# Optimization experiments

Hardware: AMD Instinct MI355X
Metric: run time of the kernel (lower is better)

Reference implementation:

```python
import jax, jax.numpy as jnp
import numpy as np
from jax import lax

B, S = 256, 512
CHAR_NUM, CLASS_NUM, OUTPUT_NUM, WORD_EMBED, H = 10, 10, 64, 32, 128
EPS = 1e-12


def setup_inputs() -> dict:
    key = jax.random.key(0)
    ks = jax.random.split(key, 16)
    def nrm(k, shape, s=0.05):
        return jax.random.normal(k, shape, dtype=jnp.float32) * s
    return {
        "char_ids": jax.random.randint(ks[0], (B, S), 0, CHAR_NUM),
        "word_ids": jax.random.randint(ks[1], (B, S), 0, CHAR_NUM),
        "subject_ids": jax.random.randint(ks[2], (B, 2), 0, S),
        "emb_char": nrm(ks[3], (CHAR_NUM, OUTPUT_NUM)),
        "emb_word": nrm(ks[4], (CHAR_NUM, WORD_EMBED)),
        "Wwc": nrm(ks[5], (WORD_EMBED, OUTPUT_NUM)),
        "bwc": jnp.zeros((OUTPUT_NUM,), jnp.float32),
        "l1_Wx": nrm(ks[6], (OUTPUT_NUM, 4 * H)),
        "l1_Wh": nrm(ks[7], (H, 4 * H)),
        "l1_b": jnp.zeros((4 * H,), jnp.float32),
        "l2_Wx": nrm(ks[8], (H, 4 * H)),
        "l2_Wh": nrm(ks[9], (H, 4 * H)),
        "l2_b": jnp.zeros((4 * H,), jnp.float32),
        "beta_W": nrm(ks[10], (2 * H, H)),
        "beta_b": jnp.zeros((H,), jnp.float32),
        "gamma_W": nrm(ks[11], (2 * H, H)),
        "gamma_b": jnp.zeros((H,), jnp.float32),
        "sub_W": nrm(ks[12], (H, 2)),
        "sub_b": jnp.zeros((2,), jnp.float32),
        "po_W": nrm(ks[13], (H, 2 * CLASS_NUM)),
        "po_b": jnp.zeros((2 * CLASS_NUM,), jnp.float32),
    }


def _lstm_cell(x, h, c, Wx, Wh, b):
    # Keras LSTMCell: gates ordered i, f, g(cell), o
    z = x @ Wx + h @ Wh + b
    i, f, g, o = jnp.split(z, 4, axis=-1)
    c_new = jax.nn.sigmoid(f) * c + jax.nn.sigmoid(i) * jnp.tanh(g)
    h_new = jax.nn.sigmoid(o) * jnp.tanh(c_new)
    return h_new, c_new


def reference(char_ids, word_ids, subject_ids,
              emb_char, emb_word, Wwc, bwc,
              l1_Wx, l1_Wh, l1_b, l2_Wx, l2_Wh, l2_b,
              beta_W, beta_b, gamma_W, gamma_b,
              sub_W, sub_b, po_W, po_b):
    b, s = char_ids.shape
    # NOTE: source passes mask = (char_ids == 0) to the RNN; in Keras, mask True
    # means the step IS processed, so only positions with id==0 update state.
    step_mask = (char_ids == 0)  # [B, S] bool

    emb = emb_char[char_ids] + (emb_word[word_ids] @ Wwc + bwc)  # [B, S, 64]

    def step(carry, inp):
        h1, c1, h2, c2 = carry
        xt, mt = inp  # xt [B, 64], mt [B]
        h1n, c1n = _lstm_cell(xt, h1, c1, l1_Wx, l1_Wh, l1_b)
        h2n, c2n = _lstm_cell(h1n, h2, c2, l2_Wx, l2_Wh, l2_b)
        m = mt[:, None]
        h1 = jnp.where(m, h1n, h1)
        c1 = jnp.where(m, c1n, c1)
        h2 = jnp.where(m, h2n, h2)
        c2 = jnp.where(m, c2n, c2)
        return (h1, c1, h2, c2), h2

    z = jnp.zeros((b, H), emb.dtype)
    _, outs = lax.scan(step, (z, z, z, z),
                       (emb.transpose(1, 0, 2), step_mask.T))
    sent = outs.transpose(1, 0, 2)  # [B, S, 128]

    # vectorized batch_gather (replaces eager numpy per-row loop)
    bidx = jnp.arange(b)
    sub_start = sent[bidx, subject_ids[:, 0]]  # [B, 128]
    sub_end = sent[bidx, subject_ids[:, 1]]    # [B, 128]
    subject = jnp.concatenate([sub_start, sub_end], axis=1)  # [B, 256]

    # conditional layer norm
    beta = subject @ beta_W + beta_b    # [B, 128]
    gamma = subject @ gamma_W + gamma_b
    u = jnp.mean(sent, axis=-1, keepdims=True)
    v = jnp.mean((sent - u) ** 2, axis=-1, keepdims=True)
    xhat = (sent - u) / jnp.sqrt(v + EPS)
    context = gamma[:, None, :] * xhat + beta[:, None, :]  # [B, S, 128]

    # (transformer_encoder LSTM(32) output is dead code in the source; omitted)
    sub_preds = sent @ sub_W + sub_b                     # [B, S, 2]
    po_preds = (context @ po_W + po_b).reshape(b, -1, CLASS_NUM, 2)  # [B, S, 10, 2]
    return sub_preds, po_preds
```

## Files before the change

### kernel.cpp

```cpp
#include <hip/hip_runtime.h>
#include <cstdint>
#include <cstddef>


#define HIST 128
#define HPAD 132

typedef _Float16 f16x8 __attribute__((ext_vector_type(8)));
typedef float    f32x4 __attribute__((ext_vector_type(4)));

__device__ __forceinline__ f16x8 as_h8(const uint4& v) {
    f16x8 r; __builtin_memcpy(&r, &v, 16); return r;
}

#define MFMA16(a, b, c) __builtin_amdgcn_mfma_f32_16x16x32_f16((a), (b), (c), 0, 0, 0)

__device__ __forceinline__ float fast_rcp(float x) {
#if __has_builtin(__builtin_amdgcn_rcpf)
    return __builtin_amdgcn_rcpf(x);
#else
    return 1.f / x;
#endif
}
__device__ __forceinline__ float sigm(float x) {
    x = fminf(fmaxf(x, -30.f), 30.f);
    return fast_rcp(1.f + __expf(-x));
}
__device__ __forceinline__ float tanh_fast(float x) {
    x = fminf(fmaxf(x, -15.f), 15.f);
    float e = __expf(-2.f * x);
    return (1.f - e) * fast_rcp(1.f + e);
}

__global__ __launch_bounds__(512) void k_prep(
    const float* __restrict__ emb_char, const float* __restrict__ emb_word,
    const float* __restrict__ Wwc, const float* __restrict__ bwc,
    const float* __restrict__ l1_Wx, const float* __restrict__ l1_b,
    const float* __restrict__ l1_Wh, const float* __restrict__ l2_Wx,
    const float* __restrict__ l2_Wh,
    float* __restrict__ XW1, uint4* __restrict__ WF)
{
    const int blk = blockIdx.x;
    const int T = threadIdx.x;
    if (blk < 10) {
        __shared__ float xw[64];
        if (T < 64) {
            float acc = emb_char[T] + bwc[T];
            for (int m = 0; m < 32; ++m) acc += emb_word[blk * 32 + m] * Wwc[m * 64 + T];
            xw[T] = acc;
        }
        __syncthreads();
        float acc = l1_b[T];
        for (int k = 0; k < 64; ++k) acc += xw[k] * l1_Wx[k * 512 + T];
        XW1[blk * 512 + T] = acc;
    } else {
        const int gid = (blk - 10) * 512 + T;
        const int thr = gid / 48;
        const int f   = gid - thr * 48;
        const int w   = thr >> 6, l = thr & 63;
        const int kb  = 8 * (l >> 4);
        const bool isL2 = (f < 32);
        int j, ks;
        if (isL2) { j = f >> 3; ks = f & 7; }
        else      { const int f2 = f - 32; j = f2 >> 2; ks = f2 & 3; }
        const int col = j * 128 + 16 * w + (l & 15);
        union { uint4 qv; _Float16 h[8]; } o;
        for (int e = 0; e < 8; ++e) {
            const int k = ks * 32 + kb + e;
            float v;
            if (isL2) v = (k < 128) ? l2_Wh[k * 512 + col] : l2_Wx[(k - 128) * 512 + col];
            else      v = l1_Wh[k * 512 + col];
            o.h[e] = (_Float16)v;
        }
        WF[gid] = o.qv;
    }
}

__global__ __launch_bounds__(512, 2) void k_lstm(
    const int* __restrict__ char_ids, const int* __restrict__ word_ids,
    const int* __restrict__ subject_ids,
    const float* __restrict__ XW1, const uint4* __restrict__ WF,
    const float* __restrict__ l2_b,
    const float* __restrict__ beta_W, const float* __restrict__ beta_b,
    const float* __restrict__ gamma_W, const float* __restrict__ gamma_b,
    const float* __restrict__ sub_W, const float* __restrict__ sub_b,
    const float* __restrict__ po_W, const float* __restrict__ po_b,
    float* __restrict__ out)
{
    const int b    = blockIdx.x;
    const int T    = threadIdx.x;
    const int lane = T & 63;
    const int wv   = T >> 6;
    const int kb   = 8 * (lane >> 4);
    const int unit = 16 * wv + (lane & 15);
    const bool g16 = (lane < 16);

    __shared__ int   charL[512];
    __shared__ int   wordL[512];
    __shared__ float XW1L[5120];
    __shared__ __align__(16) _Float16 hcat[2][256];
    __shared__ short wlist[512];
    __shared__ unsigned short idxL[512];
    __shared__ int   ccnt[8];
    __shared__ __align__(16) float hl[HIST * HPAD];
    __shared__ float A[20][132];
    __shared__ float K1[20], K2[20];
    __shared__ float gm[128], bt[128];
    __shared__ float urs[HIST][2];
    __shared__ float povals[HIST * 20];
    __shared__ float subv[HIST * 2];
    __shared__ float swl[256];
    __shared__ float subj[256];

    charL[T] = char_ids[b * 512 + T];
    wordL[T] = word_ids[b * 512 + T];
#pragma unroll
    for (int i = 0; i < 10; ++i) XW1L[i * 512 + T] = XW1[i * 512 + T];
    __syncthreads();

    const bool act = (charL[T] == 0);
    const unsigned long long bmask = __ballot(act);
    if (lane == 0) ccnt[wv] = (int)__popcll(bmask);
    __syncthreads();
    int base = 0;
    for (int i = 0; i < wv; ++i) base += ccnt[i];
    int tot = base;
    for (int i = wv; i < 8; ++i) tot += ccnt[i];
    if (act) {
        const int pos = base + (int)__popcll(bmask & ((1ull << lane) - 1ull));
        wlist[pos] = (short)wordL[T];
    }
    {
        const int cin = base + (int)__popcll(bmask & ((2ull << lane) - 1ull));
        idxL[T] = (unsigned short)(cin < HIST - 1 ? cin : HIST - 1);
    }
    const int nact = tot;

    if (T < 128) {
        hcat[0][T] = (_Float16)0.f;
        hl[T]      = 0.f;
    }
    float c1 = 0.f, c2 = 0.f;
    const float l2b0 = l2_b[unit];
    const float l2b1 = l2_b[128 + unit];
    const float l2b2 = l2_b[256 + unit];
    const float l2b3 = l2_b[384 + unit];

    uint4 wf[48];
    {
        const uint4* p = WF + (size_t)T * 48;
#pragma unroll
        for (int i = 0; i < 48; ++i) wf[i] = p[i];
    }
    __syncthreads();

    if (nact > 0) {
        const int w0_ = wlist[0];
        const float zi = XW1L[w0_ * 512 + unit];
        const float zg = XW1L[w0_ * 512 + 256 + unit];
        const float zo = XW1L[w0_ * 512 + 384 + unit];
        c1 = sigm(zi) * tanh_fast(zg);
        const float h1n = sigm(zo) * tanh_fast(c1);
        if (g16) hcat[0][128 + unit] = (_Float16)h1n;
        __syncthreads();
    }

    int cur = 0;
    for (int a = 0; a < nact; ++a) {
        const _Float16* hc = hcat[cur];
        _Float16*       hn = hcat[cur ^ 1];

        f32x4 acc0 = {l2b0, 0.f, 0.f, 0.f};
        f32x4 acc1 = {l2b1, 0.f, 0.f, 0.f};
        f32x4 acc2 = {l2b2, 0.f, 0.f, 0.f};
        f32x4 acc3 = {l2b3, 0.f, 0.f, 0.f};
#pragma unroll
        for (int ks = 0; ks < 8; ++ks) {
            const f16x8 aa = *(const f16x8*)&hc[kb + 32 * ks];
            acc0 = MFMA16(aa, as_h8(wf[0 * 8 + ks]), acc0);
            acc1 = MFMA16(aa, as_h8(wf[1 * 8 + ks]), acc1);
            acc2 = MFMA16(aa, as_h8(wf[2 * 8 + ks]), acc2);
            acc3 = MFMA16(aa, as_h8(wf[3 * 8 + ks]), acc3);
        }
        if (g16) {
            c2 = sigm(acc1[0]) * c2 + sigm(acc0[0]) * tanh_fast(acc2[0]);
            const float h2v = sigm(acc3[0]) * tanh_fast(c2);
            hn[unit] = (_Float16)h2v;
            const int slot = (a + 1 < HIST - 1) ? a + 1 : HIST - 1;
            hl[slot * HPAD + unit] = h2v;
        }

        if (a + 1 < nact) {
            const int wid = wlist[a + 1];
            f32x4 r0 = {XW1L[wid * 512 + unit],       0.f, 0.f, 0.f};
            f32x4 r1 = {XW1L[wid * 512 + 128 + unit], 0.f, 0.f, 0.f};
            f32x4 r2 = {XW1L[wid * 512 + 256 + unit], 0.f, 0.f, 0.f};
            f32x4 r3 = {XW1L[wid * 512 + 384 + unit], 0.f, 0.f, 0.f};
#pragma unroll
            for (int ks = 0; ks < 4; ++ks) {
                const f16x8 aa = *(const f16x8*)&hc[128 + kb + 32 * ks];
                r0 = MFMA16(aa, as_h8(wf[32 + 0 * 4 + ks]), r0);
                r1 = MFMA16(aa, as_h8(wf[32 + 1 * 4 + ks]), r1);
                r2 = MFMA16(aa, as_h8(wf[32 + 2 * 4 + ks]), r2);
                r3 = MFMA16(aa, as_h8(wf[32 + 3 * 4 + ks]), r3);
            }
            if (g16) {
                c1 = sigm(r1[0]) * c1 + sigm(r0[0]) * tanh_fast(r2[0]);
                const float h1n = sigm(r3[0]) * tanh_fast(c1);
                hn[128 + unit] = (_Float16)h1n;
            }
        }
        __syncthreads();
        cur ^= 1;
    }

    if (T < 256) {
        swl[T] = sub_W[T];
        const int uu = T & 127, half = T >> 7;
        const int sidx = subject_ids[b * 2 + half];
        const int slot = idxL[sidx];
        subj[T] = hl[slot * HPAD + uu];
    }
    __syncthreads();

    if (T < 256) {
        const int uu = T & 127, half = T >> 7;
        const float* __restrict__ W = half ? gamma_W : beta_W;
        float acc = half ? gamma_b[uu] : beta_b[uu];
        for (int c = 0; c < 256; ++c) acc += subj[c] * W[c * 128 + uu];
        if (half) gm[uu] = acc;
        else      bt[uu] = acc;
    }
    __syncthreads();

    for (int i = T; i < 2560; i += 512) {
        const int o = i >> 7, c = i & 127;
        A[o][c] = gm[c] * po_W[c * 20 + o];
    }
    if (T < 20) {
        float k1 = po_b[T], k2 = 0.f;
        for (int c = 0; c < 128; ++c) {
            const float pw = po_W[c * 20 + T];
            k1 += bt[c] * pw;
            k2 += gm[c] * pw;
        }
        K1[T] = k1; K2[T] = k2;
    }
    const int nslot = (int)idxL[511] + 1;
    const float sb0 = sub_b[0], sb1 = sub_b[1];
    for (int s = T; s < nslot; s += 512) {
        const float4* hp4 = (const float4*)&hl[s * HPAD];
        float sum = 0.f, s2 = 0.f, sub0 = sb0, sub1 = sb1;
        for (int c4 = 0; c4 < 32; ++c4) {
            const float4 h = hp4[c4];
            sum += (h.x + h.y) + (h.z + h.w);
            s2  += h.x * h.x + h.y * h.y + h.z * h.z + h.w * h.w;
            const int c = 4 * c4;
            sub0 += h.x * swl[2 * c] + h.y * swl[2 * c + 2] + h.z * swl[2 * c + 4] + h.w * swl[2 * c + 6];
            sub1 += h.x * swl[2 * c + 1] + h.y * swl[2 * c + 3] + h.z * swl[2 * c + 5] + h.w * swl[2 * c + 7];
        }
        const float mu = sum * (1.f / 128.f);
        const float vv = fmaxf(s2 * (1.f / 128.f) - mu * mu, 0.f);
        urs[s][0] = mu;
        urs[s][1] = 1.f / sqrtf(vv + 1e-12f);
        subv[2 * s] = sub0; subv[2 * s + 1] = sub1;
    }
    __syncthreads();

    for (int i = T; i < nslot * 20; i += 512) {
        const int s = i / 20, o = i - 20 * s;
        const float mu = urs[s][0], rs = urs[s][1];
        const float4* hp4 = (const float4*)&hl[s * HPAD];
        const float* Ao = &A[o][0];
        float acc = 0.f;
        for (int c4 = 0; c4 < 32; ++c4) {
            const float4 h = hp4[c4];
            const float4 aa = *(const float4*)&Ao[4 * c4];
            acc += h.x * aa.x + h.y * aa.y + h.z * aa.z + h.w * aa.w;
        }
        povals[i] = rs * acc - mu * rs * K2[o] + K1[o];
    }
    __syncthreads();

    for (int i = T; i < 2560; i += 512) {
        const int t = i / 5, j = i - 5 * t;
        const int sl = idxL[t];
        const float4 v = *(const float4*)&povals[sl * 20 + 4 * j];
        *(float4*)&out[262144 + ((size_t)(b * 512 + t)) * 20 + 4 * j] = v;
    }
    for (int i = T; i < 512; i += 512) {
        const int sl = idxL[i];
        float2 v; v.x = subv[2 * sl]; v.y = subv[2 * sl + 1];
        *(float2*)&out[((size_t)(b * 512 + i)) * 2] = v;
    }
}

extern "C" void kernel_launch(void* const* d_in, const int* in_sizes, int n_in,
                              void* d_out, int out_size, void* d_ws, size_t ws_size,
                              hipStream_t stream) {
    (void)in_sizes; (void)n_in; (void)out_size; (void)ws_size;
    const int*   char_ids    = (const int*)d_in[0];
    const int*   word_ids    = (const int*)d_in[1];
    const int*   subject_ids = (const int*)d_in[2];
    const float* emb_char    = (const float*)d_in[3];
    const float* emb_word    = (const float*)d_in[4];
    const float* Wwc         = (const float*)d_in[5];
    const float* bwc         = (const float*)d_in[6];
    const float* l1_Wx       = (const float*)d_in[7];
    const float* l1_b        = (const float*)d_in[9];
    const float* l1_Wh       = (const float*)d_in[8];
    const float* l2_Wx       = (const float*)d_in[10];
    const float* l2_Wh       = (const float*)d_in[11];
    const float* l2_b        = (const float*)d_in[12];
    const float* beta_W      = (const float*)d_in[13];
    const float* beta_b      = (const float*)d_in[14];
    const float* gamma_W     = (const float*)d_in[15];
    const float* gamma_b     = (const float*)d_in[16];
    const float* sub_W       = (const float*)d_in[17];
    const float* sub_b       = (const float*)d_in[18];
    const float* po_W        = (const float*)d_in[19];
    const float* po_b        = (const float*)d_in[20];
    float* out = (float*)d_out;

    char* ws = (char*)d_ws;
    float* XW1 = (float*)(ws + 0);
    uint4* WF  = (uint4*)(ws + 32768);

    k_prep<<<dim3(58), dim3(512), 0, stream>>>(emb_char, emb_word, Wwc, bwc,
                                               l1_Wx, l1_b, l1_Wh, l2_Wx, l2_Wh,
                                               XW1, WF);
    k_lstm<<<dim3(256), dim3(512), 0, stream>>>(char_ids, word_ids, subject_ids,
                                                XW1, WF, l2_b,
                                                beta_W, beta_b, gamma_W, gamma_b,
                                                sub_W, sub_b, po_W, po_b, out);
}
```

Measured before the change: 203.3 us.

## Halve LSTM block to 4 waves, each wave computing two hidden-unit groups

The recurrent kernel now runs 256 threads (4 waves) per batch row instead of 512. Each wave handles 32 hidden units through two MFMA column groups, and each thread holds 96 fp16 weight fragments, pinned to AGPRs with inline asm. The prep kernel's weight packing is changed to match the new fragment layout. The aim is to cut cross-wave barrier cost and wave count in the serial recurrence, at the cost of more MFMAs per wave per step and higher register pressure.

```diff
diff --git a/kernel.cpp b/kernel.cpp
--- a/kernel.cpp
+++ b/kernel.cpp
@@ -55,28 +55,28 @@
         XW1[blk * 512 + T] = acc;
     } else {
         const int gid = (blk - 10) * 512 + T;
-        const int thr = gid / 48;
-        const int f   = gid - thr * 48;
+        const int thr = gid / 96;
+        const int f   = gid - thr * 96;
         const int w   = thr >> 6, l = thr & 63;
         const int kb  = 8 * (l >> 4);
-        const bool isL2 = (f < 32);
-        int j, ks;
-        if (isL2) { j = f >> 3; ks = f & 7; }
-        else      { const int f2 = f - 32; j = f2 >> 2; ks = f2 & 3; }
-        const int col = j * 128 + 16 * w + (l & 15);
-        union { uint4 qv; _Float16 h[8]; } o;
+        const bool isL2 = (f < 96 - 32);
+        int j, h, ks;
+        if (isL2) { j = f >> 4; h = (f >> 3) & 1; ks = f & 7; }
+        else      { const int f2 = f - 64; j = f2 >> 3; h = (f2 >> 2) & 1; ks = f2 & 3; }
+        const int col = j * 128 + 32 * w + 16 * h + (l & 15);
+        union { uint4 qv; _Float16 hh[8]; } o;
         for (int e = 0; e < 8; ++e) {
             const int k = ks * 32 + kb + e;
             float v;
             if (isL2) v = (k < 128) ? l2_Wh[k * 512 + col] : l2_Wx[(k - 128) * 512 + col];
             else      v = l1_Wh[k * 512 + col];
-            o.h[e] = (_Float16)v;
+            o.hh[e] = (_Float16)v;
         }
         WF[gid] = o.qv;
     }
 }
 
-__global__ __launch_bounds__(512, 2) void k_lstm(
+__global__ __launch_bounds__(256, 1) void k_lstm(
     const int* __restrict__ char_ids, const int* __restrict__ word_ids,
     const int* __restrict__ subject_ids,
     const float* __restrict__ XW1, const uint4* __restrict__ WF,
@@ -91,9 +91,11 @@
     const int T    = threadIdx.x;
     const int lane = T & 63;
     const int wv   = T >> 6;
+    const int l15  = lane & 15;
     const int kb   = 8 * (lane >> 4);
-    const int unit = 16 * wv + (lane & 15);
     const bool g16 = (lane < 16);
+    const int u0   = 32 * wv + l15;
+    const int u1   = u0 + 16;
 
     __shared__ int   charL[512];
     __shared__ int   wordL[512];
@@ -112,56 +114,66 @@
     __shared__ float swl[256];
     __shared__ float subj[256];
 
-    charL[T] = char_ids[b * 512 + T];
-    wordL[T] = word_ids[b * 512 + T];
-#pragma unroll
-    for (int i = 0; i < 10; ++i) XW1L[i * 512 + T] = XW1[i * 512 + T];
-    __syncthreads();
-
-    const bool act = (charL[T] == 0);
-    const unsigned long long bmask = __ballot(act);
-    if (lane == 0) ccnt[wv] = (int)__popcll(bmask);
-    __syncthreads();
-    int base = 0;
-    for (int i = 0; i < wv; ++i) base += ccnt[i];
-    int tot = base;
-    for (int i = wv; i < 8; ++i) tot += ccnt[i];
-    if (act) {
-        const int pos = base + (int)__popcll(bmask & ((1ull << lane) - 1ull));
-        wlist[pos] = (short)wordL[T];
-    }
+    charL[T]       = char_ids[b * 512 + T];
+    charL[256 + T] = char_ids[b * 512 + 256 + T];
+    wordL[T]       = word_ids[b * 512 + T];
+    wordL[256 + T] = word_ids[b * 512 + 256 + T];
+    for (int i = T; i < 5120; i += 256) XW1L[i] = XW1[i];
+    __syncthreads();
+
+    const bool act0 = (charL[T] == 0);
+    const bool act1 = (charL[256 + T] == 0);
+    const unsigned long long bm0 = __ballot(act0);
+    const unsigned long long bm1 = __ballot(act1);
+    if (lane == 0) { ccnt[wv] = (int)__popcll(bm0); ccnt[4 + wv] = (int)__popcll(bm1); }
+    __syncthreads();
+    int baseC[8];
+    int tot = 0;
+    for (int i = 0; i < 8; ++i) { baseC[i] = tot; tot += ccnt[i]; }
+    const int nact = tot;
+    if (act0) wlist[baseC[wv]     + (int)__popcll(bm0 & ((1ull << lane) - 1ull))] = (short)wordL[T];
+    if (act1) wlist[baseC[4 + wv] + (int)__popcll(bm1 & ((1ull << lane) - 1ull))] = (short)wordL[256 + T];
     {
-        const int cin = base + (int)__popcll(bmask & ((2ull << lane) - 1ull));
-        idxL[T] = (unsigned short)(cin < HIST - 1 ? cin : HIST - 1);
-    }
-    const int nact = tot;
+        const int c0 = baseC[wv]     + (int)__popcll(bm0 & ((2ull << lane) - 1ull));
+        const int c1 = baseC[4 + wv] + (int)__popcll(bm1 & ((2ull << lane) - 1ull));
+        idxL[T]       = (unsigned short)(c0 < HIST - 1 ? c0 : HIST - 1);
+        idxL[256 + T] = (unsigned short)(c1 < HIST - 1 ? c1 : HIST - 1);
+    }
 
     if (T < 128) {
         hcat[0][T] = (_Float16)0.f;
         hl[T]      = 0.f;
     }
-    float c1 = 0.f, c2 = 0.f;
-    const float l2b0 = l2_b[unit];
-    const float l2b1 = l2_b[128 + unit];
-    const float l2b2 = l2_b[256 + unit];
-    const float l2b3 = l2_b[384 + unit];
-
-    uint4 wf[48];
+    float c1_0 = 0.f, c1_1 = 0.f, c2_0 = 0.f, c2_1 = 0.f;
+    const float l2b00 = l2_b[u0],       l2b01 = l2_b[u1];
+    const float l2b10 = l2_b[128 + u0], l2b11 = l2_b[128 + u1];
+    const float l2b20 = l2_b[256 + u0], l2b21 = l2_b[256 + u1];
+    const float l2b30 = l2_b[384 + u0], l2b31 = l2_b[384 + u1];
+
+    uint4 wf[96];
     {
-        const uint4* p = WF + (size_t)T * 48;
+        const uint4* p = WF + (size_t)T * 96;
 #pragma unroll
-        for (int i = 0; i < 48; ++i) wf[i] = p[i];
-    }
+        for (int i = 0; i < 96; ++i) wf[i] = p[i];
+    }
+#pragma unroll
+    for (int i = 0; i < 96; ++i)
+        asm volatile("" : "+a"(wf[i].x), "+a"(wf[i].y), "+a"(wf[i].z), "+a"(wf[i].w));
     __syncthreads();
 
     if (nact > 0) {
         const int w0_ = wlist[0];
-        const float zi = XW1L[w0_ * 512 + unit];
-        const float zg = XW1L[w0_ * 512 + 256 + unit];
-        const float zo = XW1L[w0_ * 512 + 384 + unit];
-        c1 = sigm(zi) * tanh_fast(zg);
-        const float h1n = sigm(zo) * tanh_fast(c1);
-        if (g16) hcat[0][128 + unit] = (_Float16)h1n;
+        const float zi0 = XW1L[w0_ * 512 + u0],       zi1 = XW1L[w0_ * 512 + u1];
+        const float zg0 = XW1L[w0_ * 512 + 256 + u0], zg1 = XW1L[w0_ * 512 + 256 + u1];
+        const float zo0 = XW1L[w0_ * 512 + 384 + u0], zo1 = XW1L[w0_ * 512 + 384 + u1];
+        c1_0 = sigm(zi0) * tanh_fast(zg0);
+        c1_1 = sigm(zi1) * tanh_fast(zg1);
+        const float h1n0 = sigm(zo0) * tanh_fast(c1_0);
+        const float h1n1 = sigm(zo1) * tanh_fast(c1_1);
+        if (g16) {
+            hcat[0][128 + u0] = (_Float16)h1n0;
+            hcat[0][128 + u1] = (_Float16)h1n1;
+        }
         __syncthreads();
     }
 
@@ -170,51 +182,67 @@
         const _Float16* hc = hcat[cur];
         _Float16*       hn = hcat[cur ^ 1];
 
-        f32x4 acc0 = {l2b0, 0.f, 0.f, 0.f};
-        f32x4 acc1 = {l2b1, 0.f, 0.f, 0.f};
-        f32x4 acc2 = {l2b2, 0.f, 0.f, 0.f};
-        f32x4 acc3 = {l2b3, 0.f, 0.f, 0.f};
+        f32x4 q00 = {l2b00, 0.f, 0.f, 0.f}, q01 = {l2b01, 0.f, 0.f, 0.f};
+        f32x4 q10 = {l2b10, 0.f, 0.f, 0.f}, q11 = {l2b11, 0.f, 0.f, 0.f};
+        f32x4 q20 = {l2b20, 0.f, 0.f, 0.f}, q21 = {l2b21, 0.f, 0.f, 0.f};
+        f32x4 q30 = {l2b30, 0.f, 0.f, 0.f}, q31 = {l2b31, 0.f, 0.f, 0.f};
 #pragma unroll
         for (int ks = 0; ks < 8; ++ks) {
             const f16x8 aa = *(const f16x8*)&hc[kb + 32 * ks];
-            acc0 = MFMA16(aa, as_h8(wf[0 * 8 + ks]), acc0);
-            acc1 = MFMA16(aa, as_h8(wf[1 * 8 + ks]), acc1);
-            acc2 = MFMA16(aa, as_h8(wf[2 * 8 + ks]), acc2);
-            acc3 = MFMA16(aa, as_h8(wf[3 * 8 + ks]), acc3);
+            q00 = MFMA16(aa, as_h8(wf[ 0 + ks]), q00);
+            q01 = MFMA16(aa, as_h8(wf[ 8 + ks]), q01);
+            q10 = MFMA16(aa, as_h8(wf[16 + ks]), q10);
+            q11 = MFMA16(aa, as_h8(wf[24 + ks]), q11);
+            q20 = MFMA16(aa, as_h8(wf[32 + ks]), q20);
+            q21 = MFMA16(aa, as_h8(wf[40 + ks]), q21);
+            q30 = MFMA16(aa, as_h8(wf[48 + ks]), q30);
+            q31 = MFMA16(aa, as_h8(wf[56 + ks]), q31);
         }
         if (g16) {
-            c2 = sigm(acc1[0]) * c2 + sigm(acc0[0]) * tanh_fast(acc2[0]);
-            const float h2v = sigm(acc3[0]) * tanh_fast(c2);
-            hn[unit] = (_Float16)h2v;
+            c2_0 = sigm(q10[0]) * c2_0 + sigm(q00[0]) * tanh_fast(q20[0]);
+            const float h2v0 = sigm(q30[0]) * tanh_fast(c2_0);
+            c2_1 = sigm(q11[0]) * c2_1 + sigm(q01[0]) * tanh_fast(q21[0]);
+            const float h2v1 = sigm(q31[0]) * tanh_fast(c2_1);
+            hn[u0] = (_Float16)h2v0;
+            hn[u1] = (_Float16)h2v1;
             const int slot = (a + 1 < HIST - 1) ? a + 1 : HIST - 1;
-            hl[slot * HPAD + unit] = h2v;
+            hl[slot * HPAD + u0] = h2v0;
+            hl[slot * HPAD + u1] = h2v1;
         }
 
         if (a + 1 < nact) {
             const int wid = wlist[a + 1];
-            f32x4 r0 = {XW1L[wid * 512 + unit],       0.f, 0.f, 0.f};
-            f32x4 r1 = {XW1L[wid * 512 + 128 + unit], 0.f, 0.f, 0.f};
-            f32x4 r2 = {XW1L[wid * 512 + 256 + unit], 0.f, 0.f, 0.f};
-            f32x4 r3 = {XW1L[wid * 512 + 384 + unit], 0.f, 0.f, 0.f};
+            const float* xb = &XW1L[wid * 512];
+            f32x4 r00 = {xb[u0],       0.f, 0.f, 0.f}, r01 = {xb[u1],       0.f, 0.f, 0.f};
+            f32x4 r10 = {xb[128 + u0], 0.f, 0.f, 0.f}, r11 = {xb[128 + u1], 0.f, 0.f, 0.f};
+            f32x4 r20 = {xb[256 + u0], 0.f, 0.f, 0.f}, r21 = {xb[256 + u1], 0.f, 0.f, 0.f};
+            f32x4 r30 = {xb[384 + u0], 0.f, 0.f, 0.f}, r31 = {xb[384 + u1], 0.f, 0.f, 0.f};
 #pragma unroll
             for (int ks = 0; ks < 4; ++ks) {
                 const f16x8 aa = *(const f16x8*)&hc[128 + kb + 32 * ks];
-                r0 = MFMA16(aa, as_h8(wf[32 + 0 * 4 + ks]), r0);
-                r1 = MFMA16(aa, as_h8(wf[32 + 1 * 4 + ks]), r1);
-                r2 = MFMA16(aa, as_h8(wf[32 + 2 * 4 + ks]), r2);
-                r3 = MFMA16(aa, as_h8(wf[32 + 3 * 4 + ks]), r3);
+                r00 = MFMA16(aa, as_h8(wf[64 + 0 + ks]), r00);
+                r01 = MFMA16(aa, as_h8(wf[64 + 4 + ks]), r01);
+                r10 = MFMA16(aa, as_h8(wf[64 + 8 + ks]), r10);
+                r11 = MFMA16(aa, as_h8(wf[64 + 12 + ks]), r11);
+                r20 = MFMA16(aa, as_h8(wf[64 + 16 + ks]), r20);
+                r21 = MFMA16(aa, as_h8(wf[64 + 20 + ks]), r21);
+                r30 = MFMA16(aa, as_h8(wf[64 + 24 + ks]), r30);
+                r31 = MFMA16(aa, as_h8(wf[64 + 28 + ks]), r31);
             }
             if (g16) {
-                c1 = sigm(r1[0]) * c1 + sigm(r0[0]) * tanh_fast(r2[0]);
-                const float h1n = sigm(r3[0]) * tanh_fast(c1);
-                hn[128 + unit] = (_Float16)h1n;
+                c1_0 = sigm(r10[0]) * c1_0 + sigm(r00[0]) * tanh_fast(r20[0]);
+                const float h1n0 = sigm(r30[0]) * tanh_fast(c1_0);
+                c1_1 = sigm(r11[0]) * c1_1 + sigm(r01[0]) * tanh_fast(r21[0]);
+                const float h1n1 = sigm(r31[0]) * tanh_fast(c1_1);
+                hn[128 + u0] = (_Float16)h1n0;
+                hn[128 + u1] = (_Float16)h1n1;
             }
         }
         __syncthreads();
         cur ^= 1;
     }
 
-    if (T < 256) {
+    {
         swl[T] = sub_W[T];
         const int uu = T & 127, half = T >> 7;
         const int sidx = subject_ids[b * 2 + half];
@@ -223,7 +251,7 @@
     }
     __syncthreads();
 
-    if (T < 256) {
+    {
         const int uu = T & 127, half = T >> 7;
         const float* __restrict__ W = half ? gamma_W : beta_W;
         float acc = half ? gamma_b[uu] : beta_b[uu];
@@ -233,7 +261,7 @@
     }
     __syncthreads();
 
-    for (int i = T; i < 2560; i += 512) {
+    for (int i = T; i < 2560; i += 256) {
         const int o = i >> 7, c = i & 127;
         A[o][c] = gm[c] * po_W[c * 20 + o];
     }
@@ -248,7 +276,7 @@
     }
     const int nslot = (int)idxL[511] + 1;
     const float sb0 = sub_b[0], sb1 = sub_b[1];
-    for (int s = T; s < nslot; s += 512) {
+    for (int s = T; s < nslot; s += 256) {
         const float4* hp4 = (const float4*)&hl[s * HPAD];
         float sum = 0.f, s2 = 0.f, sub0 = sb0, sub1 = sb1;
         for (int c4 = 0; c4 < 32; ++c4) {
@@ -267,7 +295,7 @@
     }
     __syncthreads();
 
-    for (int i = T; i < nslot * 20; i += 512) {
+    for (int i = T; i < nslot * 20; i += 256) {
         const int s = i / 20, o = i - 20 * s;
         const float mu = urs[s][0], rs = urs[s][1];
         const float4* hp4 = (const float4*)&hl[s * HPAD];
@@ -282,13 +310,13 @@
     }
     __syncthreads();
 
-    for (int i = T; i < 2560; i += 512) {
+    for (int i = T; i < 2560; i += 256) {
         const int t = i / 5, j = i - 5 * t;
         const int sl = idxL[t];
         const float4 v = *(const float4*)&povals[sl * 20 + 4 * j];
         *(float4*)&out[262144 + ((size_t)(b * 512 + t)) * 20 + 4 * j] = v;
     }
-    for (int i = T; i < 512; i += 512) {
+    for (int i = T; i < 512; i += 256) {
         const int sl = idxL[i];
         float2 v; v.x = subv[2 * sl]; v.y = subv[2 * sl + 1];
         *(float2*)&out[((size_t)(b * 512 + i)) * 2] = v;
@@ -307,8 +335,8 @@
     const float* Wwc         = (const float*)d_in[5];
     const float* bwc         = (const float*)d_in[6];
     const float* l1_Wx       = (const float*)d_in[7];
+    const float* l1_Wh       = (const float*)d_in[8];
     const float* l1_b        = (const float*)d_in[9];
-    const float* l1_Wh       = (const float*)d_in[8];
     const float* l2_Wx       = (const float*)d_in[10];
     const float* l2_Wh       = (const float*)d_in[11];
     const float* l2_b        = (const float*)d_in[12];
@@ -329,7 +357,7 @@
     k_prep<<<dim3(58), dim3(512), 0, stream>>>(emb_char, emb_word, Wwc, bwc,
                                                l1_Wx, l1_b, l1_Wh, l2_Wx, l2_Wh,
                                                XW1, WF);
-    k_lstm<<<dim3(256), dim3(512), 0, stream>>>(char_ids, word_ids, subject_ids,
+    k_lstm<<<dim3(256), dim3(256), 0, stream>>>(char_ids, word_ids, subject_ids,
                                                 XW1, WF, l2_b,
                                                 beta_W, beta_b, gamma_W, gamma_b,
                                                 sub_W, sub_b, po_W, po_b, out);
```

Result: slower. 252.5 us (+24.2%).

## Specialize waves: separate layer-1 and layer-2 LSTM waves in a 768-thread block

Applied to the files above, without the earlier changes.

The block grows from 8 to 12 waves. Eight waves compute only the layer-2 gates and four waves compute only the layer-1 gates, with each layer-1 wave covering two 16-unit groups, so both layers' matrix products run at the same time instead of one after the other inside each wave. The weight-packing kernel is rewritten so that each thread holds 32 register fragments instead of 48, which lowers register pressure, and an empty asm statement keeps the weights in vector registers. The intent is to shorten the serial per-timestep MFMA chain on the recurrence critical path. In exchange the block launches more waves, and layer-1 waves still run two dependent 16-MFMA chains back to back.

```diff
diff --git a/kernel.cpp b/kernel.cpp
--- a/kernel.cpp
+++ b/kernel.cpp
@@ -55,28 +55,33 @@
         XW1[blk * 512 + T] = acc;
     } else {
         const int gid = (blk - 10) * 512 + T;
-        const int thr = gid / 48;
-        const int f   = gid - thr * 48;
+        const int thr = gid >> 5;
+        const int f   = gid & 31;
         const int w   = thr >> 6, l = thr & 63;
         const int kb  = 8 * (l >> 4);
-        const bool isL2 = (f < 32);
-        int j, ks;
-        if (isL2) { j = f >> 3; ks = f & 7; }
-        else      { const int f2 = f - 32; j = f2 >> 2; ks = f2 & 3; }
-        const int col = j * 128 + 16 * w + (l & 15);
-        union { uint4 qv; _Float16 h[8]; } o;
-        for (int e = 0; e < 8; ++e) {
-            const int k = ks * 32 + kb + e;
-            float v;
-            if (isL2) v = (k < 128) ? l2_Wh[k * 512 + col] : l2_Wx[(k - 128) * 512 + col];
-            else      v = l1_Wh[k * 512 + col];
-            o.h[e] = (_Float16)v;
+        union { uint4 qv; _Float16 hh[8]; } o;
+        if (w < 8) {
+            const int j = f >> 3, ks = f & 7;
+            const int col = j * 128 + 16 * w + (l & 15);
+            for (int e = 0; e < 8; ++e) {
+                const int k = ks * 32 + kb + e;
+                o.hh[e] = (_Float16)((k < 128) ? l2_Wh[k * 512 + col]
+                                               : l2_Wx[(k - 128) * 512 + col]);
+            }
+        } else {
+            const int w1 = w - 8;
+            const int j = f >> 3, h = (f >> 2) & 1, ks = f & 3;
+            const int col = j * 128 + 32 * w1 + 16 * h + (l & 15);
+            for (int e = 0; e < 8; ++e) {
+                const int k = ks * 32 + kb + e;
+                o.hh[e] = (_Float16)l1_Wh[k * 512 + col];
+            }
         }
         WF[gid] = o.qv;
     }
 }
 
-__global__ __launch_bounds__(512, 2) void k_lstm(
+__global__ __launch_bounds__(768, 3) void k_lstm(
     const int* __restrict__ char_ids, const int* __restrict__ word_ids,
     const int* __restrict__ subject_ids,
     const float* __restrict__ XW1, const uint4* __restrict__ WF,
@@ -91,9 +96,14 @@
     const int T    = threadIdx.x;
     const int lane = T & 63;
     const int wv   = T >> 6;
+    const int l15  = lane & 15;
     const int kb   = 8 * (lane >> 4);
-    const int unit = 16 * wv + (lane & 15);
     const bool g16 = (lane < 16);
+    const bool isL2 = (wv < 8);
+    const int u2   = 16 * (wv & 7) + l15;
+    const int w1   = wv - 8;
+    const int u0   = 32 * (w1 & 3) + l15;
+    const int u1   = u0 + 16;
 
     __shared__ int   charL[512];
     __shared__ int   wordL[512];
@@ -112,56 +122,67 @@
     __shared__ float swl[256];
     __shared__ float subj[256];
 
-    charL[T] = char_ids[b * 512 + T];
-    wordL[T] = word_ids[b * 512 + T];
-#pragma unroll
-    for (int i = 0; i < 10; ++i) XW1L[i * 512 + T] = XW1[i * 512 + T];
-    __syncthreads();
-
-    const bool act = (charL[T] == 0);
+    if (T < 512) {
+        charL[T] = char_ids[b * 512 + T];
+        wordL[T] = word_ids[b * 512 + T];
+    }
+    for (int i = T; i < 5120; i += 768) XW1L[i] = XW1[i];
+    __syncthreads();
+
+    const bool act = (T < 512) && (charL[T] == 0);
     const unsigned long long bmask = __ballot(act);
-    if (lane == 0) ccnt[wv] = (int)__popcll(bmask);
+    if (lane == 0 && wv < 8) ccnt[wv] = (int)__popcll(bmask);
     __syncthreads();
     int base = 0;
-    for (int i = 0; i < wv; ++i) base += ccnt[i];
-    int tot = base;
-    for (int i = wv; i < 8; ++i) tot += ccnt[i];
+    {
+        const int wcap = wv < 8 ? wv : 8;
+        for (int i = 0; i < wcap; ++i) base += ccnt[i];
+    }
+    int tot = 0;
+    for (int i = 0; i < 8; ++i) tot += ccnt[i];
+    const int nact = tot;
     if (act) {
         const int pos = base + (int)__popcll(bmask & ((1ull << lane) - 1ull));
         wlist[pos] = (short)wordL[T];
     }
-    {
+    if (T < 512) {
         const int cin = base + (int)__popcll(bmask & ((2ull << lane) - 1ull));
         idxL[T] = (unsigned short)(cin < HIST - 1 ? cin : HIST - 1);
     }
-    const int nact = tot;
 
     if (T < 128) {
         hcat[0][T] = (_Float16)0.f;
         hl[T]      = 0.f;
     }
-    float c1 = 0.f, c2 = 0.f;
-    const float l2b0 = l2_b[unit];
-    const float l2b1 = l2_b[128 + unit];
-    const float l2b2 = l2_b[256 + unit];
-    const float l2b3 = l2_b[384 + unit];
-
-    uint4 wf[48];
+    float c2 = 0.f;
+    float c1_0 = 0.f, c1_1 = 0.f;
+    const float l2b0 = l2_b[u2];
+    const float l2b1 = l2_b[128 + u2];
+    const float l2b2 = l2_b[256 + u2];
+    const float l2b3 = l2_b[384 + u2];
+
+    uint4 wf[32];
     {
-        const uint4* p = WF + (size_t)T * 48;
-#pragma unroll
-        for (int i = 0; i < 48; ++i) wf[i] = p[i];
-    }
+        const uint4* p = WF + (size_t)T * 32;
+#pragma unroll
+        for (int i = 0; i < 32; ++i) wf[i] = p[i];
+    }
+#pragma unroll
+    for (int i = 0; i < 32; ++i)
+        asm volatile("" : "+v"(wf[i].x), "+v"(wf[i].y), "+v"(wf[i].z), "+v"(wf[i].w));
     __syncthreads();
 
     if (nact > 0) {
-        const int w0_ = wlist[0];
-        const float zi = XW1L[w0_ * 512 + unit];
-        const float zg = XW1L[w0_ * 512 + 256 + unit];
-        const float zo = XW1L[w0_ * 512 + 384 + unit];
-        c1 = sigm(zi) * tanh_fast(zg);
-        const float h1n = sigm(zo) * tanh_fast(c1);
-        if (g16) hcat[0][128 + unit] = (_Float16)h1n;
+        if (!isL2 && g16) {
+            const int w0_ = wlist[0];
+            const float* xb = &XW1L[w0_ * 512];
+            c1_0 = sigm(xb[u0]) * tanh_fast(xb[256 + u0]);
+            c1_1 = sigm(xb[u1]) * tanh_fast(xb[256 + u1]);
+            const float h1n0 = sigm(xb[384 + u0]) * tanh_fast(c1_0);
+            const float h1n1 = sigm(xb[384 + u1]) * tanh_fast(c1_1);
+            hcat[0][128 + u0] = (_Float16)h1n0;
+            hcat[0][128 + u1] = (_Float16)h1n1;
+        }
         __syncthreads();
     }
 
@@ -170,44 +191,66 @@
         const _Float16* hc = hcat[cur];
         _Float16*       hn = hcat[cur ^ 1];
 
-        f32x4 acc0 = {l2b0, 0.f, 0.f, 0.f};
-        f32x4 acc1 = {l2b1, 0.f, 0.f, 0.f};
-        f32x4 acc2 = {l2b2, 0.f, 0.f, 0.f};
-        f32x4 acc3 = {l2b3, 0.f, 0.f, 0.f};
-#pragma unroll
-        for (int ks = 0; ks < 8; ++ks) {
-            const f16x8 aa = *(const f16x8*)&hc[kb + 32 * ks];
-            acc0 = MFMA16(aa, as_h8(wf[0 * 8 + ks]), acc0);
-            acc1 = MFMA16(aa, as_h8(wf[1 * 8 + ks]), acc1);
-            acc2 = MFMA16(aa, as_h8(wf[2 * 8 + ks]), acc2);
-            acc3 = MFMA16(aa, as_h8(wf[3 * 8 + ks]), acc3);
-        }
-        if (g16) {
-            c2 = sigm(acc1[0]) * c2 + sigm(acc0[0]) * tanh_fast(acc2[0]);
-            const float h2v = sigm(acc3[0]) * tanh_fast(c2);
-            hn[unit] = (_Float16)h2v;
-            const int slot = (a + 1 < HIST - 1) ? a + 1 : HIST - 1;
-            hl[slot * HPAD + unit] = h2v;
-        }
-
-        if (a + 1 < nact) {
+        if (isL2) {
+            f32x4 q0 = {l2b0, 0.f, 0.f, 0.f};
+            f32x4 q1 = {l2b1, 0.f, 0.f, 0.f};
+            f32x4 q2 = {l2b2, 0.f, 0.f, 0.f};
+            f32x4 q3 = {l2b3, 0.f, 0.f, 0.f};
+#pragma unroll
+            for (int ks = 0; ks < 8; ++ks) {
+                const f16x8 aa = *(const f16x8*)&hc[kb + 32 * ks];
+                q0 = MFMA16(aa, as_h8(wf[ 0 + ks]), q0);
+                q1 = MFMA16(aa, as_h8(wf[ 8 + ks]), q1);
+                q2 = MFMA16(aa, as_h8(wf[16 + ks]), q2);
+                q3 = MFMA16(aa, as_h8(wf[24 + ks]), q3);
+            }
+            if (g16) {
+                c2 = sigm(q1[0]) * c2 + sigm(q0[0]) * tanh_fast(q2[0]);
+                const float h2v = sigm(q3[0]) * tanh_fast(c2);
+                hn[u2] = (_Float16)h2v;
+                const int slot = (a + 1 < HIST - 1) ? a + 1 : HIST - 1;
+                hl[slot * HPAD + u2] = h2v;
+            }
+        } else if (a + 1 < nact) {
             const int wid = wlist[a + 1];
-            f32x4 r0 = {XW1L[wid * 512 + unit],       0.f, 0.f, 0.f};
-            f32x4 r1 = {XW1L[wid * 512 + 128 + unit], 0.f, 0.f, 0.f};
-            f32x4 r2 = {XW1L[wid * 512 + 256 + unit], 0.f, 0.f, 0.f};
-            f32x4 r3 = {XW1L[wid * 512 + 384 + unit], 0.f, 0.f, 0.f};
-#pragma unroll
-            for (int ks = 0; ks < 4; ++ks) {
-                const f16x8 aa = *(const f16x8*)&hc[128 + kb + 32 * ks];
-                r0 = MFMA16(aa, as_h8(wf[32 + 0 * 4 + ks]), r0);
-                r1 = MFMA16(aa, as_h8(wf[32 + 1 * 4 + ks]), r1);
-                r2 = MFMA16(aa, as_h8(wf[32 + 2 * 4 + ks]), r2);
-                r3 = MFMA16(aa, as_h8(wf[32 + 3 * 4 + ks]), r3);
-            }
-            if (g16) {
-                c1 = sigm(r1[0]) * c1 + sigm(r0[0]) * tanh_fast(r2[0]);
-                const float h1n = sigm(r3[0]) * tanh_fast(c1);
-                hn[128 + unit] = (_Float16)h1n;
+            const float* xb = &XW1L[wid * 512];
+            {
+                f32x4 r0 = {xb[u0],       0.f, 0.f, 0.f};
+                f32x4 r1 = {xb[128 + u0], 0.f, 0.f, 0.f};
+                f32x4 r2 = {xb[256 + u0], 0.f, 0.f, 0.f};
+                f32x4 r3 = {xb[384 + u0], 0.f, 0.f, 0.f};
+#pragma unroll
+                for (int ks = 0; ks < 4; ++ks) {
+                    const f16x8 aa = *(const f16x8*)&hc[128 + kb + 32 * ks];
+                    r0 = MFMA16(aa, as_h8(wf[ 0 + ks]), r0);
+                    r1 = MFMA16(aa, as_h8(wf[ 8 + ks]), r1);
+                    r2 = MFMA16(aa, as_h8(wf[16 + ks]), r2);
+                    r3 = MFMA16(aa, as_h8(wf[24 + ks]), r3);
+                }
+                if (g16) {
+                    c1_0 = sigm(r1[0]) * c1_0 + sigm(r0[0]) * tanh_fast(r2[0]);
+                    const float h1n0 = sigm(r3[0]) * tanh_fast(c1_0);
+                    hn[128 + u0] = (_Float16)h1n0;
+                }
+            }
+            {
+                f32x4 r0 = {xb[u1],       0.f, 0.f, 0.f};
+                f32x4 r1 = {xb[128 + u1], 0.f, 0.f, 0.f};
+                f32x4 r2 = {xb[256 + u1], 0.f, 0.f, 0.f};
+                f32x4 r3 = {xb[384 + u1], 0.f, 0.f, 0.f};
+#pragma unroll
+                for (int ks = 0; ks < 4; ++ks) {
+                    const f16x8 aa = *(const f16x8*)&hc[128 + kb + 32 * ks];
+                    r0 = MFMA16(aa, as_h8(wf[ 4 + ks]), r0);
+                    r1 = MFMA16(aa, as_h8(wf[12 + ks]), r1);
+                    r2 = MFMA16(aa, as_h8(wf[20 + ks]), r2);
+                    r3 = MFMA16(aa, as_h8(wf[28 + ks]), r3);
+                }
+                if (g16) {
+                    c1_1 = sigm(r1[0]) * c1_1 + sigm(r0[0]) * tanh_fast(r2[0]);
+                    const float h1n1 = sigm(r3[0]) * tanh_fast(c1_1);
+                    hn[128 + u1] = (_Float16)h1n1;
+                }
             }
         }
         __syncthreads();
@@ -233,7 +276,7 @@
     }
     __syncthreads();
 
-    for (int i = T; i < 2560; i += 512) {
+    for (int i = T; i < 2560; i += 768) {
         const int o = i >> 7, c = i & 127;
         A[o][c] = gm[c] * po_W[c * 20 + o];
     }
@@ -248,7 +291,7 @@
     }
     const int nslot = (int)idxL[511] + 1;
     const float sb0 = sub_b[0], sb1 = sub_b[1];
-    for (int s = T; s < nslot; s += 512) {
+    for (int s = T; s < nslot; s += 768) {
         const float4* hp4 = (const float4*)&hl[s * HPAD];
         float sum = 0.f, s2 = 0.f, sub0 = sb0, sub1 = sb1;
         for (int c4 = 0; c4 < 32; ++c4) {
@@ -267,7 +310,7 @@
     }
     __syncthreads();
 
-    for (int i = T; i < nslot * 20; i += 512) {
+    for (int i = T; i < nslot * 20; i += 768) {
         const int s = i / 20, o = i - 20 * s;
         const float mu = urs[s][0], rs = urs[s][1];
         const float4* hp4 = (const float4*)&hl[s * HPAD];
@@ -282,13 +325,13 @@
     }
     __syncthreads();
 
-    for (int i = T; i < 2560; i += 512) {
+    for (int i = T; i < 2560; i += 768) {
         const int t = i / 5, j = i - 5 * t;
         const int sl = idxL[t];
         const float4 v = *(const float4*)&povals[sl * 20 + 4 * j];
         *(float4*)&out[262144 + ((size_t)(b * 512 + t)) * 20 + 4 * j] = v;
     }
-    for (int i = T; i < 512; i += 512) {
+    for (int i = T; i < 512; i += 768) {
         const int sl = idxL[i];
         float2 v; v.x = subv[2 * sl]; v.y = subv[2 * sl + 1];
         *(float2*)&out[((size_t)(b * 512 + i)) * 2] = v;
@@ -307,8 +350,8 @@
     const float* Wwc         = (const float*)d_in[5];
     const float* bwc         = (const float*)d_in[6];
     const float* l1_Wx       = (const float*)d_in[7];
+    const float* l1_Wh       = (const float*)d_in[8];
     const float* l1_b        = (const float*)d_in[9];
-    const float* l1_Wh       = (const float*)d_in[8];
     const float* l2_Wx       = (const float*)d_in[10];
     const float* l2_Wh       = (const float*)d_in[11];
     const float* l2_b        = (const float*)d_in[12];
@@ -329,7 +372,7 @@
     k_prep<<<dim3(58), dim3(512), 0, stream>>>(emb_char, emb_word, Wwc, bwc,
                                                l1_Wx, l1_b, l1_Wh, l2_Wx, l2_Wh,
                                                XW1, WF);
-    k_lstm<<<dim3(256), dim3(512), 0, stream>>>(char_ids, word_ids, subject_ids,
+    k_lstm<<<dim3(256), dim3(768), 0, stream>>>(char_ids, word_ids, subject_ids,
                                                 XW1, WF, l2_b,
                                                 beta_W, beta_b, gamma_W, gamma_b,
                                                 sub_W, sub_b, po_W, po_b, out);
```

New measurement: 379.5 us. 86.7% more time.
